# Optimization experiments

Hardware: AMD Instinct MI355X
Metric: run time of the kernel (lower is better)

## Reference

```python
import jax, jax.numpy as jnp
import numpy as np

B = 16384      # batch
D_IN = 512     # dim_input
K = 8          # number of cascade stages
W_STAGE = 256  # neurons added per stage
D_OUT = 128    # dim_output
EPS = 1e-5     # BatchNorm1d default eps


def setup_inputs() -> dict:
    key = jax.random.key(0)
    ks = jax.random.split(key, K + 2)
    inp = {"x": jax.random.normal(ks[0], (B, D_IN), jnp.float32)}
    d = D_IN
    for i in range(K):
        # Kaiming-ish scaling so activations stay sane through the cascade
        inp[f"W{i}"] = jax.random.normal(ks[1 + i], (W_STAGE, d), jnp.float32) * (1.0 / np.sqrt(d))
        d += W_STAGE
    inp["b"] = jnp.zeros((K, W_STAGE), jnp.float32)
    inp["gamma"] = jnp.ones((K, W_STAGE), jnp.float32)
    inp["beta"] = jnp.zeros((K, W_STAGE), jnp.float32)
    inp["Wout"] = jax.random.normal(ks[K + 1], (D_OUT, d), jnp.float32) * 0.02
    inp["bout"] = jnp.zeros((D_OUT,), jnp.float32)
    return inp


def reference(x, W0, W1, W2, W3, W4, W5, W6, W7, b, gamma, beta, Wout, bout):
    Ws = [W0, W1, W2, W3, W4, W5, W6, W7]
    feats = x
    for i in range(K):  # structural loop over fixed cascade depth
        # Linear -> ReLU
        h = jnp.maximum(feats @ Ws[i].T + b[i], 0.0)          # [B, W_STAGE]
        # BatchNorm1d (training mode: batch stats, biased variance)
        mu = h.mean(axis=0)
        var = h.var(axis=0)
        hn = (h - mu) * jax.lax.rsqrt(var + EPS)
        feats = jnp.concatenate([feats, hn * gamma[i] + beta[i]], axis=1)
    return feats @ Wout.T + bout
```

## Files before the change

kernel.cpp:

```cpp
#include <hip/hip_runtime.h>
#include <hip/hip_bf16.h>

typedef __attribute__((ext_vector_type(8))) __bf16 bf16x8;
typedef __attribute__((ext_vector_type(4))) __bf16 bf16x4;
typedef __attribute__((ext_vector_type(4))) float f32x4;

#define B_ROWS 16384
#define LDF 2560
#define BN_EPS 1e-5f

__device__ __forceinline__ void async16(void* lds, const void* g) {
  __builtin_amdgcn_global_load_lds(
      (const __attribute__((address_space(1))) unsigned int*)g,
      (__attribute__((address_space(3))) unsigned int*)lds, 16, 0, 0);
}

__device__ __forceinline__ bf16x8 cvt8(float4 a, float4 b) {
  bf16x8 t;
  t[0] = (__bf16)a.x; t[1] = (__bf16)a.y; t[2] = (__bf16)a.z; t[3] = (__bf16)a.w;
  t[4] = (__bf16)b.x; t[5] = (__bf16)b.y; t[6] = (__bf16)b.z; t[7] = (__bf16)b.w;
  return t;
}

__global__ __launch_bounds__(512) void gemm_stage(
    const __bf16* __restrict__ A, const __bf16* __restrict__ W,
    const float* __restrict__ badj,
    __bf16* __restrict__ hout, float* __restrict__ Cpart,
    float* __restrict__ colsum, float* __restrict__ colsumsq,
    int Kd, int Ksplit, int mode, int bxbits, int skbits)
{
  __shared__ __bf16 lds[3][12288];

  const int tid  = threadIdx.x;
  const int lane = tid & 63;
  const int wid  = tid >> 6;
  const int wm   = wid >> 2, wn = wid & 3;
  const int fr   = lane & 15, fk = lane >> 4;

  const int cpx  = gridDim.x >> 3;
  const int wgid = (blockIdx.x & 7) * cpx + (blockIdx.x >> 3);
  const int bx   = wgid & ((1 << bxbits) - 1);
  const int sk   = (wgid >> bxbits) & ((1 << skbits) - 1);
  const int by   = wgid >> (bxbits + skbits);
  const int bn0  = bx * 128, bm0 = by * 64;
  const int k0   = sk * Ksplit;

  const int srow = tid >> 3;
  const int sko  = ((tid & 7) ^ (srow & 7)) << 3;
  const __bf16* a0p = A + (size_t)(bm0 + srow) * LDF + k0 + sko;
  const __bf16* b0p = W + (size_t)(bn0 + srow) * Kd + k0 + sko;
  const __bf16* b1p = b0p + (size_t)64 * Kd;

#define STAGE(b, kt) do {                                            \
    async16((void*)(&lds[b][(size_t)tid * 8]),          a0p + (kt)); \
    async16((void*)(&lds[b][(size_t)(4096 + tid * 8)]), b0p + (kt)); \
    async16((void*)(&lds[b][(size_t)(8192 + tid * 8)]), b1p + (kt)); \
  } while (0)

  int aoff[2][2], boff[2][2];
#pragma unroll
  for (int ksub = 0; ksub < 2; ++ksub) {
    const int kc = ksub * 4 + fk;
#pragma unroll
    for (int i = 0; i < 2; ++i) {
      int ra = wm * 32 + i * 16 + fr;
      aoff[ksub][i] = ra * 64 + ((kc ^ (ra & 7)) << 3);
      int rb2 = wn * 32 + i * 16 + fr;
      boff[ksub][i] = 4096 + rb2 * 64 + ((kc ^ (rb2 & 7)) << 3);
    }
  }

  f32x4 acc[2][2] = {};

  const int NT = Ksplit >> 6;
  STAGE(0, 0);
  STAGE(1, 64);

  int rb = 0;
  for (int t = 0; t < NT; ++t) {
    if (t < NT - 1) asm volatile("s_waitcnt vmcnt(3)" ::: "memory");
    else            asm volatile("s_waitcnt vmcnt(0)" ::: "memory");
    __builtin_amdgcn_s_barrier();
    __builtin_amdgcn_sched_barrier(0);

    if (t + 2 < NT) {
      int sb = rb + 2; if (sb >= 3) sb -= 3;
      STAGE(sb, (t + 2) * 64);
    }
    __builtin_amdgcn_sched_barrier(0);

    const __bf16* bp = lds[rb];
#pragma unroll
    for (int ksub = 0; ksub < 2; ++ksub) {
      bf16x8 af[2], bf[2];
#pragma unroll
      for (int i = 0; i < 2; ++i) {
        af[i] = *(const bf16x8*)(bp + aoff[ksub][i]);
        bf[i] = *(const bf16x8*)(bp + boff[ksub][i]);
      }
#pragma unroll
      for (int mi = 0; mi < 2; ++mi)
#pragma unroll
        for (int ni = 0; ni < 2; ++ni)
          acc[mi][ni] = __builtin_amdgcn_mfma_f32_16x16x32_bf16(af[mi], bf[ni], acc[mi][ni], 0, 0, 0);
    }

    if (++rb == 3) rb = 0;
  }
#undef STAGE

  if (mode) {
    float psum[2] = {0.f, 0.f}, psq[2] = {0.f, 0.f};
#pragma unroll
    for (int mi = 0; mi < 2; ++mi) {
#pragma unroll
      for (int ni = 0; ni < 2; ++ni) {
        const int col  = bn0 + wn * 32 + ni * 16 + fr;
        const int row0 = bm0 + wm * 32 + mi * 16 + fk * 4;
        const float bv = badj[col];
        __bf16* hp = hout + (size_t)row0 * LDF + col;
#pragma unroll
        for (int r = 0; r < 4; ++r) {
          float v = fmaxf(acc[mi][ni][r] + bv, 0.f);
          psum[ni] += v; psq[ni] += v * v;
          hp[(size_t)r * LDF] = (__bf16)v;
        }
      }
    }
#pragma unroll
    for (int ni = 0; ni < 2; ++ni) {
      float s = psum[ni], q = psq[ni];
      s += __shfl_xor(s, 16); s += __shfl_xor(s, 32);
      q += __shfl_xor(q, 16); q += __shfl_xor(q, 32);
      if (fk == 0) {
        int col = bn0 + wn * 32 + ni * 16 + fr;
        atomicAdd(&colsum[col], s);
        atomicAdd(&colsumsq[col], q);
      }
    }
  } else {
    float* Cp = Cpart + (size_t)sk * B_ROWS * 128;
#pragma unroll
    for (int mi = 0; mi < 2; ++mi) {
#pragma unroll
      for (int ni = 0; ni < 2; ++ni) {
        const int col  = bn0 + wn * 32 + ni * 16 + fr;
        const int row0 = bm0 + wm * 32 + mi * 16 + fk * 4;
        float* cp = Cp + (size_t)row0 * 128 + col;
#pragma unroll
        for (int r = 0; r < 4; ++r)
          cp[(size_t)r * 128] = acc[mi][ni][r];
      }
    }
  }
}

__global__ __launch_bounds__(256) void epi_final(
    const float* __restrict__ Cp, const float* __restrict__ badj,
    float* __restrict__ out)
{
  int idx = blockIdx.x * 256 + threadIdx.x;
  int r = idx >> 5, c = (idx & 31) * 4;
  const float* p = Cp + (size_t)r * 128 + c;
  const size_t pl = (size_t)B_ROWS * 128;
  float4 a = *(const float4*)p;
  float4 b = *(const float4*)(p + pl);
  float4 d2 = *(const float4*)(p + 2 * pl);
  float4 e = *(const float4*)(p + 3 * pl);
  float4 bv = *(const float4*)(badj + c);
  float4 o;
  o.x = a.x + b.x + d2.x + e.x + bv.x;
  o.y = a.y + b.y + d2.y + e.y + bv.y;
  o.z = a.z + b.z + d2.z + e.z + bv.z;
  o.w = a.w + b.w + d2.w + e.w + bv.w;
  *(float4*)(out + (size_t)r * 128 + c) = o;
}

__global__ void cast_x_kernel(const float* __restrict__ x, __bf16* __restrict__ feats) {
  int idx = blockIdx.x * blockDim.x + threadIdx.x;
  int row = idx >> 6, c8 = (idx & 63) << 3;
  const float4* xp = (const float4*)(x + (size_t)row * 512 + c8);
  float4 a = xp[0], b = xp[1];
  *(bf16x8*)(feats + (size_t)row * LDF + c8) = cvt8(a, b);
}

__global__ void prep_w(const float* __restrict__ W, const float* __restrict__ bias,
                       const float* __restrict__ colsum, const float* __restrict__ colsumsq,
                       const float* __restrict__ gamma, const float* __restrict__ beta,
                       __bf16* __restrict__ Wb, float* __restrict__ badj, int Kd)
{
  const int n = blockIdx.x, t = threadIdx.x;
  const float invB = 1.0f / 16384.0f;
  float accb = 0.f;
  for (int c0 = t * 4; c0 < Kd; c0 += 1024) {
    float4 w = *(const float4*)(W + (size_t)n * Kd + c0);
    float wv[4] = {w.x, w.y, w.z, w.w};
    bf16x4 o;
#pragma unroll
    for (int i = 0; i < 4; ++i) {
      int c = c0 + i;
      float sc = 1.f, sh = 0.f;
      if (c >= 512) {
        int idx = c - 512;
        float mu  = colsum[idx] * invB;
        float var = colsumsq[idx] * invB - mu * mu;
        sc = gamma[idx] * rsqrtf(var + BN_EPS);
        sh = beta[idx] - mu * sc;
      }
      accb += wv[i] * sh;
      o[i] = (__bf16)(wv[i] * sc);
    }
    *(bf16x4*)(Wb + (size_t)n * Kd + c0) = o;
  }
  __shared__ float red[256];
  red[t] = accb;
  __syncthreads();
  for (int s = 128; s > 0; s >>= 1) {
    if (t < s) red[t] += red[t + s];
    __syncthreads();
  }
  if (t == 0) badj[n] = bias[n] + red[0];
}

extern "C" void kernel_launch(void* const* d_in, const int* in_sizes, int n_in,
                              void* d_out, int out_size, void* d_ws, size_t ws_size,
                              hipStream_t stream) {
  const float* x = (const float*)d_in[0];
  const float* Wi[8];
  for (int i = 0; i < 8; ++i) Wi[i] = (const float*)d_in[1 + i];
  const float* b     = (const float*)d_in[9];
  const float* gamma = (const float*)d_in[10];
  const float* beta  = (const float*)d_in[11];
  const float* Wout  = (const float*)d_in[12];
  const float* bout  = (const float*)d_in[13];
  float* out = (float*)d_out;

  char* ws = (char*)d_ws;
  __bf16* feats = (__bf16*)ws;
  size_t off = (size_t)B_ROWS * LDF * 2;
  __bf16* wb[8];
  {
    int d = 512;
    for (int i = 0; i < 8; ++i) { wb[i] = (__bf16*)(ws + off); off += (size_t)256 * d * 2; d += 256; }
  }
  __bf16* woutb = (__bf16*)(ws + off); off += (size_t)128 * 2560 * 2;
  float* Cpart    = (float*)(ws + off); off += (size_t)4 * B_ROWS * 128 * 4;
  float* colsum   = (float*)(ws + off); off += 8 * 256 * 4;
  float* colsumsq = (float*)(ws + off); off += 8 * 256 * 4;
  float* badj     = (float*)(ws + off); off += 9 * 256 * 4;

  hipMemsetAsync(colsum, 0, 2 * 8 * 256 * 4, stream);

  cast_x_kernel<<<B_ROWS * 64 / 256, 256, 0, stream>>>(x, feats);

  int d = 512;
  for (int i = 0; i < 8; ++i) {
    prep_w<<<256, 256, 0, stream>>>(Wi[i], b + i * 256, colsum, colsumsq,
                                    gamma, beta, wb[i], badj + i * 256, d);
    gemm_stage<<<512, 512, 0, stream>>>(feats, wb[i], badj + i * 256,
                                        feats + d, nullptr,
                                        colsum + i * 256, colsumsq + i * 256,
                                        d, d, 1, 1, 0);
    d += 256;
  }
  prep_w<<<128, 256, 0, stream>>>(Wout, bout, colsum, colsumsq,
                                  gamma, beta, woutb, badj + 8 * 256, 2560);
  gemm_stage<<<1024, 512, 0, stream>>>(feats, woutb, nullptr,
                                       nullptr, Cpart, nullptr, nullptr,
                                       2560, 640, 0, 0, 2);
  epi_final<<<2048, 256, 0, stream>>>(Cpart, badj + 8 * 256, out);
}
```

Measured before the change: 292.9 us.

## Load A fragments directly from global into registers, drop memset via prep_w zeroing

The A tile in the GEMM is no longer staged through LDS. Each wave loads its MFMA A fragments straight from global memory into registers at every k-step, which shrinks LDS use and cuts the async copy count per stage from three to two. The separate hipMemsetAsync is removed; each stage's prep_w kernel now zeroes its own colsum/colsumsq slice before the GEMM accumulates into it. The trade-off is that A is read from global without cross-wave sharing, and the load latency now sits right before the MFMAs with no prefetch.

```diff
diff --git a/kernel.cpp b/kernel.cpp
--- a/kernel.cpp
+++ b/kernel.cpp
@@ -29,7 +29,7 @@
     float* __restrict__ colsum, float* __restrict__ colsumsq,
     int Kd, int Ksplit, int mode, int bxbits, int skbits)
 {
-  __shared__ __bf16 lds[3][12288];
+  __shared__ __bf16 lds[3][8192];
 
   const int tid  = threadIdx.x;
   const int lane = tid & 63;
@@ -47,26 +47,30 @@
 
   const int srow = tid >> 3;
   const int sko  = ((tid & 7) ^ (srow & 7)) << 3;
-  const __bf16* a0p = A + (size_t)(bm0 + srow) * LDF + k0 + sko;
   const __bf16* b0p = W + (size_t)(bn0 + srow) * Kd + k0 + sko;
   const __bf16* b1p = b0p + (size_t)64 * Kd;
 
 #define STAGE(b, kt) do {                                            \
-    async16((void*)(&lds[b][(size_t)tid * 8]),          a0p + (kt)); \
-    async16((void*)(&lds[b][(size_t)(4096 + tid * 8)]), b0p + (kt)); \
-    async16((void*)(&lds[b][(size_t)(8192 + tid * 8)]), b1p + (kt)); \
+    async16((void*)(&lds[b][(size_t)tid * 8]),          b0p + (kt)); \
+    async16((void*)(&lds[b][(size_t)(4096 + tid * 8)]), b1p + (kt)); \
   } while (0)
 
-  int aoff[2][2], boff[2][2];
+  const __bf16* aF[2][2];
+#pragma unroll
+  for (int ksub = 0; ksub < 2; ++ksub)
+#pragma unroll
+    for (int i = 0; i < 2; ++i)
+      aF[ksub][i] = A + (size_t)(bm0 + wm * 32 + i * 16 + fr) * LDF
+                      + k0 + (ksub * 4 + fk) * 8;
+
+  int boff[2][2];
 #pragma unroll
   for (int ksub = 0; ksub < 2; ++ksub) {
     const int kc = ksub * 4 + fk;
 #pragma unroll
     for (int i = 0; i < 2; ++i) {
-      int ra = wm * 32 + i * 16 + fr;
-      aoff[ksub][i] = ra * 64 + ((kc ^ (ra & 7)) << 3);
-      int rb2 = wn * 32 + i * 16 + fr;
-      boff[ksub][i] = 4096 + rb2 * 64 + ((kc ^ (rb2 & 7)) << 3);
+      int r = wn * 32 + i * 16 + fr;
+      boff[ksub][i] = r * 64 + ((kc ^ (r & 7)) << 3);
     }
   }
 
@@ -78,11 +82,19 @@
 
   int rb = 0;
   for (int t = 0; t < NT; ++t) {
-    if (t < NT - 1) asm volatile("s_waitcnt vmcnt(3)" ::: "memory");
+    if (t < NT - 1) asm volatile("s_waitcnt vmcnt(2)" ::: "memory");
     else            asm volatile("s_waitcnt vmcnt(0)" ::: "memory");
     __builtin_amdgcn_s_barrier();
     __builtin_amdgcn_sched_barrier(0);
 
+    bf16x8 af[2][2];
+#pragma unroll
+    for (int ksub = 0; ksub < 2; ++ksub)
+#pragma unroll
+      for (int i = 0; i < 2; ++i)
+        af[ksub][i] = *(const bf16x8*)(aF[ksub][i] + (size_t)t * 64);
+    __builtin_amdgcn_sched_barrier(0);
+
     if (t + 2 < NT) {
       int sb = rb + 2; if (sb >= 3) sb -= 3;
       STAGE(sb, (t + 2) * 64);
@@ -92,17 +104,15 @@
     const __bf16* bp = lds[rb];
 #pragma unroll
     for (int ksub = 0; ksub < 2; ++ksub) {
-      bf16x8 af[2], bf[2];
-#pragma unroll
-      for (int i = 0; i < 2; ++i) {
-        af[i] = *(const bf16x8*)(bp + aoff[ksub][i]);
+      bf16x8 bf[2];
+#pragma unroll
+      for (int i = 0; i < 2; ++i)
         bf[i] = *(const bf16x8*)(bp + boff[ksub][i]);
-      }
 #pragma unroll
       for (int mi = 0; mi < 2; ++mi)
 #pragma unroll
         for (int ni = 0; ni < 2; ++ni)
-          acc[mi][ni] = __builtin_amdgcn_mfma_f32_16x16x32_bf16(af[mi], bf[ni], acc[mi][ni], 0, 0, 0);
+          acc[mi][ni] = __builtin_amdgcn_mfma_f32_16x16x32_bf16(af[ksub][mi], bf[ni], acc[mi][ni], 0, 0, 0);
     }
 
     if (++rb == 3) rb = 0;
@@ -187,9 +197,11 @@
 __global__ void prep_w(const float* __restrict__ W, const float* __restrict__ bias,
                        const float* __restrict__ colsum, const float* __restrict__ colsumsq,
                        const float* __restrict__ gamma, const float* __restrict__ beta,
-                       __bf16* __restrict__ Wb, float* __restrict__ badj, int Kd)
+                       __bf16* __restrict__ Wb, float* __restrict__ badj, int Kd,
+                       float* __restrict__ zs, float* __restrict__ zq)
 {
   const int n = blockIdx.x, t = threadIdx.x;
+  if (zs && t == 0 && n < 256) { zs[n] = 0.f; zq[n] = 0.f; }
   const float invB = 1.0f / 16384.0f;
   float accb = 0.f;
   for (int c0 = t * 4; c0 < Kd; c0 += 1024) {
@@ -249,14 +261,13 @@
   float* colsumsq = (float*)(ws + off); off += 8 * 256 * 4;
   float* badj     = (float*)(ws + off); off += 9 * 256 * 4;
 
-  hipMemsetAsync(colsum, 0, 2 * 8 * 256 * 4, stream);
-
   cast_x_kernel<<<B_ROWS * 64 / 256, 256, 0, stream>>>(x, feats);
 
   int d = 512;
   for (int i = 0; i < 8; ++i) {
     prep_w<<<256, 256, 0, stream>>>(Wi[i], b + i * 256, colsum, colsumsq,
-                                    gamma, beta, wb[i], badj + i * 256, d);
+                                    gamma, beta, wb[i], badj + i * 256, d,
+                                    colsum + i * 256, colsumsq + i * 256);
     gemm_stage<<<512, 512, 0, stream>>>(feats, wb[i], badj + i * 256,
                                         feats + d, nullptr,
                                         colsum + i * 256, colsumsq + i * 256,
@@ -264,7 +275,8 @@
     d += 256;
   }
   prep_w<<<128, 256, 0, stream>>>(Wout, bout, colsum, colsumsq,
-                                  gamma, beta, woutb, badj + 8 * 256, 2560);
+                                  gamma, beta, woutb, badj + 8 * 256, 2560,
+                                  nullptr, nullptr);
   gemm_stage<<<1024, 512, 0, stream>>>(feats, woutb, nullptr,
                                        nullptr, Cpart, nullptr, nullptr,
                                        2560, 640, 0, 0, 2);
```

Result: slower. 553.3 us (+88.9%).

## Drop split-K in final GEMM, fuse bias epilogue, zero stats in prep_w

Applied to the files above, without the earlier changes.

The final output GEMM no longer splits K four ways into partial buffers. Each of 256 workgroups now computes the full K=2560 reduction and writes output plus bias directly, which removes the epi_final kernel and the 32MB partial-sum round trip. The memset of BN statistics is folded into prep_w, and s_setprio is raised around the MFMA block. The risk is that the final GEMM launches only 256 workgroups, so on a chip with 256 CUs it runs as a single wave with long serial K loops.

```diff
diff --git a/kernel.cpp b/kernel.cpp
--- a/kernel.cpp
+++ b/kernel.cpp
@@ -25,9 +25,9 @@
 __global__ __launch_bounds__(512) void gemm_stage(
     const __bf16* __restrict__ A, const __bf16* __restrict__ W,
     const float* __restrict__ badj,
-    __bf16* __restrict__ hout, float* __restrict__ Cpart,
+    __bf16* __restrict__ hout, float* __restrict__ fout,
     float* __restrict__ colsum, float* __restrict__ colsumsq,
-    int Kd, int Ksplit, int mode, int bxbits, int skbits)
+    int Kd, int mode, int bxbits)
 {
   __shared__ __bf16 lds[3][12288];
 
@@ -40,15 +40,13 @@
   const int cpx  = gridDim.x >> 3;
   const int wgid = (blockIdx.x & 7) * cpx + (blockIdx.x >> 3);
   const int bx   = wgid & ((1 << bxbits) - 1);
-  const int sk   = (wgid >> bxbits) & ((1 << skbits) - 1);
-  const int by   = wgid >> (bxbits + skbits);
+  const int by   = wgid >> bxbits;
   const int bn0  = bx * 128, bm0 = by * 64;
-  const int k0   = sk * Ksplit;
 
   const int srow = tid >> 3;
   const int sko  = ((tid & 7) ^ (srow & 7)) << 3;
-  const __bf16* a0p = A + (size_t)(bm0 + srow) * LDF + k0 + sko;
-  const __bf16* b0p = W + (size_t)(bn0 + srow) * Kd + k0 + sko;
+  const __bf16* a0p = A + (size_t)(bm0 + srow) * LDF + sko;
+  const __bf16* b0p = W + (size_t)(bn0 + srow) * Kd + sko;
   const __bf16* b1p = b0p + (size_t)64 * Kd;
 
 #define STAGE(b, kt) do {                                            \
@@ -72,7 +70,7 @@
 
   f32x4 acc[2][2] = {};
 
-  const int NT = Ksplit >> 6;
+  const int NT = Kd >> 6;
   STAGE(0, 0);
   STAGE(1, 64);
 
@@ -90,6 +88,7 @@
     __builtin_amdgcn_sched_barrier(0);
 
     const __bf16* bp = lds[rb];
+    __builtin_amdgcn_s_setprio(1);
 #pragma unroll
     for (int ksub = 0; ksub < 2; ++ksub) {
       bf16x8 af[2], bf[2];
@@ -104,6 +103,7 @@
         for (int ni = 0; ni < 2; ++ni)
           acc[mi][ni] = __builtin_amdgcn_mfma_f32_16x16x32_bf16(af[mi], bf[ni], acc[mi][ni], 0, 0, 0);
     }
+    __builtin_amdgcn_s_setprio(0);
 
     if (++rb == 3) rb = 0;
   }
@@ -139,41 +139,20 @@
       }
     }
   } else {
-    float* Cp = Cpart + (size_t)sk * B_ROWS * 128;
 #pragma unroll
     for (int mi = 0; mi < 2; ++mi) {
 #pragma unroll
       for (int ni = 0; ni < 2; ++ni) {
         const int col  = bn0 + wn * 32 + ni * 16 + fr;
         const int row0 = bm0 + wm * 32 + mi * 16 + fk * 4;
-        float* cp = Cp + (size_t)row0 * 128 + col;
+        const float bv = badj[col];
+        float* cp = fout + (size_t)row0 * 128 + col;
 #pragma unroll
         for (int r = 0; r < 4; ++r)
-          cp[(size_t)r * 128] = acc[mi][ni][r];
-      }
-    }
-  }
-}
-
-__global__ __launch_bounds__(256) void epi_final(
-    const float* __restrict__ Cp, const float* __restrict__ badj,
-    float* __restrict__ out)
-{
-  int idx = blockIdx.x * 256 + threadIdx.x;
-  int r = idx >> 5, c = (idx & 31) * 4;
-  const float* p = Cp + (size_t)r * 128 + c;
-  const size_t pl = (size_t)B_ROWS * 128;
-  float4 a = *(const float4*)p;
-  float4 b = *(const float4*)(p + pl);
-  float4 d2 = *(const float4*)(p + 2 * pl);
-  float4 e = *(const float4*)(p + 3 * pl);
-  float4 bv = *(const float4*)(badj + c);
-  float4 o;
-  o.x = a.x + b.x + d2.x + e.x + bv.x;
-  o.y = a.y + b.y + d2.y + e.y + bv.y;
-  o.z = a.z + b.z + d2.z + e.z + bv.z;
-  o.w = a.w + b.w + d2.w + e.w + bv.w;
-  *(float4*)(out + (size_t)r * 128 + c) = o;
+          cp[(size_t)r * 128] = acc[mi][ni][r] + bv;
+      }
+    }
+  }
 }
 
 __global__ void cast_x_kernel(const float* __restrict__ x, __bf16* __restrict__ feats) {
@@ -187,9 +166,11 @@
 __global__ void prep_w(const float* __restrict__ W, const float* __restrict__ bias,
                        const float* __restrict__ colsum, const float* __restrict__ colsumsq,
                        const float* __restrict__ gamma, const float* __restrict__ beta,
-                       __bf16* __restrict__ Wb, float* __restrict__ badj, int Kd)
+                       __bf16* __restrict__ Wb, float* __restrict__ badj, int Kd,
+                       float* __restrict__ zs, float* __restrict__ zq)
 {
   const int n = blockIdx.x, t = threadIdx.x;
+  if (zs && t == 0 && n < 256) { zs[n] = 0.f; zq[n] = 0.f; }
   const float invB = 1.0f / 16384.0f;
   float accb = 0.f;
   for (int c0 = t * 4; c0 < Kd; c0 += 1024) {
@@ -244,29 +225,27 @@
     for (int i = 0; i < 8; ++i) { wb[i] = (__bf16*)(ws + off); off += (size_t)256 * d * 2; d += 256; }
   }
   __bf16* woutb = (__bf16*)(ws + off); off += (size_t)128 * 2560 * 2;
-  float* Cpart    = (float*)(ws + off); off += (size_t)4 * B_ROWS * 128 * 4;
   float* colsum   = (float*)(ws + off); off += 8 * 256 * 4;
   float* colsumsq = (float*)(ws + off); off += 8 * 256 * 4;
   float* badj     = (float*)(ws + off); off += 9 * 256 * 4;
 
-  hipMemsetAsync(colsum, 0, 2 * 8 * 256 * 4, stream);
-
   cast_x_kernel<<<B_ROWS * 64 / 256, 256, 0, stream>>>(x, feats);
 
   int d = 512;
   for (int i = 0; i < 8; ++i) {
     prep_w<<<256, 256, 0, stream>>>(Wi[i], b + i * 256, colsum, colsumsq,
-                                    gamma, beta, wb[i], badj + i * 256, d);
+                                    gamma, beta, wb[i], badj + i * 256, d,
+                                    colsum + i * 256, colsumsq + i * 256);
     gemm_stage<<<512, 512, 0, stream>>>(feats, wb[i], badj + i * 256,
                                         feats + d, nullptr,
                                         colsum + i * 256, colsumsq + i * 256,
-                                        d, d, 1, 1, 0);
+                                        d, 1, 1);
     d += 256;
   }
   prep_w<<<128, 256, 0, stream>>>(Wout, bout, colsum, colsumsq,
-                                  gamma, beta, woutb, badj + 8 * 256, 2560);
-  gemm_stage<<<1024, 512, 0, stream>>>(feats, woutb, nullptr,
-                                       nullptr, Cpart, nullptr, nullptr,
-                                       2560, 640, 0, 0, 2);
-  epi_final<<<2048, 256, 0, stream>>>(Cpart, badj + 8 * 256, out);
-}
+                                  gamma, beta, woutb, badj + 8 * 256, 2560,
+                                  nullptr, nullptr);
+  gemm_stage<<<256, 512, 0, stream>>>(feats, woutb, badj + 8 * 256,
+                                      nullptr, out, nullptr, nullptr,
+                                      2560, 0, 0);
+}
```

Measured after the change: 286.2 us. -2.3%, faster.
